# Kernel optimization log

Hardware: AMD Instinct MI355X
Metric: run time of the kernel (lower is better)

The kernel has to match this reference:

```python
import jax, jax.numpy as jnp
import numpy as np

N = 100000
E = 3200000
IN_C, H1, H2 = 512, 64, 32


def gcn_norm(edge_index, edge_weight, num_nodes):
    """PyG gcn_norm with add_self_loops=True: D^-1/2 (A+I) D^-1/2 edge weights."""
    row, col = edge_index[0], edge_index[1]
    loop = jnp.arange(num_nodes, dtype=edge_index.dtype)
    row = jnp.concatenate([row, loop])
    col = jnp.concatenate([col, loop])
    w = jnp.concatenate([edge_weight, jnp.ones((num_nodes,), edge_weight.dtype)])
    deg = jax.ops.segment_sum(w, col, num_segments=num_nodes)
    dinv = jnp.where(deg > 0, jax.lax.rsqrt(jnp.maximum(deg, 1e-12)), 0.0)
    wnorm = dinv[row] * w * dinv[col]
    return row, col, wnorm


def gcn_conv(x, W, b, row, col, wnorm, num_nodes):
    h = x @ W                                   # [N, out] linear first (out <= in)
    msg = wnorm[:, None] * h[row]               # gather + per-edge scale  [E+N, out]
    out = jax.ops.segment_sum(msg, col, num_segments=num_nodes)
    return out + b


def setup_inputs() -> dict:
    key = jax.random.key(0)
    ks = jax.random.split(key, 9)
    x = jax.random.normal(ks[0], (N, IN_C), dtype=jnp.float32)
    edge_index = jax.random.randint(ks[1], (2, E), 0, N, dtype=jnp.int64)
    edge_weight = jax.random.uniform(ks[2], (E,), dtype=jnp.float32)
    # Glorot-style init for GCN linear weights, zero bias (PyG defaults).
    def glorot(k, fan_in, fan_out):
        s = np.sqrt(6.0 / (fan_in + fan_out)).astype(np.float32)
        return jax.random.uniform(k, (fan_in, fan_out), jnp.float32, -s, s)
    return {
        "x": x,
        "edge_index": edge_index,
        "edge_weight": edge_weight,
        "W1": glorot(ks[3], IN_C, H1), "b1": jnp.zeros((H1,), jnp.float32),
        "W2": glorot(ks[4], H1, H2),  "b2": jnp.zeros((H2,), jnp.float32),
        "W3": glorot(ks[5], H2, 1),   "b3": jnp.zeros((1,), jnp.float32),
    }


def reference(x, edge_index, edge_weight, W1, b1, W2, b2, W3, b3):
    # Inference mode: dropout is identity (training=False).
    row, col, wnorm = gcn_norm(edge_index, edge_weight, N)  # cached=True: shared across layers
    h = jax.nn.relu(gcn_conv(x, W1, b1, row, col, wnorm, N))
    h = jax.nn.relu(gcn_conv(h, W2, b2, row, col, wnorm, N))
    h = gcn_conv(h, W3, b3, row, col, wnorm, N)
    return h.reshape(-1)  # [N]
```

## Files before the change

### kernel.cpp

```cpp
#include <hip/hip_runtime.h>

constexpr int BLK = 256;
constexpr int NBLKBIN = 512;
constexpr int MAXNB   = 1024;

typedef __bf16 bf16x8 __attribute__((ext_vector_type(8)));
typedef float  f32x4  __attribute__((ext_vector_type(4)));

__device__ __forceinline__ float blo(unsigned u) { return __uint_as_float(u << 16); }
__device__ __forceinline__ float bhi(unsigned u) { return __uint_as_float(u & 0xffff0000u); }

__device__ __forceinline__ int detect64(const void* ei) {
    const int* p = (const int*)ei;
    int is64 = 1;
#pragma unroll
    for (int i = 0; i < 16; ++i)
        if (p[2 * i + 1] != 0) is64 = 0;
    return is64;
}

__device__ __forceinline__ int load_idx(const void* ei, size_t pos, int is64) {
    if (is64) return (int)((const long long*)ei)[pos];
    return ((const int*)ei)[pos];
}

__global__ void k_prep(const float* __restrict__ W1, const float* __restrict__ W2,
                       __bf16* __restrict__ Wtf, __bf16* __restrict__ Wtf2,
                       int* __restrict__ bkt_cnt, int nb) {
    const int b = blockIdx.x;
    const int t = threadIdx.x;
    if (b < 16) {
        int i = b * 256 + t;
        int lane = i & 63;
        int tt   = (i >> 6) & 3;
        int k0c  = i >> 8;
        int col  = tt * 16 + (lane & 15);
        int kbase = k0c * 32 + (lane >> 4) * 8;
        bf16x8 v;
#pragma unroll
        for (int j = 0; j < 8; ++j) v[j] = (__bf16)W1[(size_t)(kbase + j) * 64 + col];
        *(bf16x8*)(Wtf + (size_t)i * 8) = v;
    } else if (b == 16) {
        int i = t;
        int lane = i & 63;
        int ct   = i >> 6;
        int tt = ct & 1, chunk = ct >> 1;
        int col  = tt * 16 + (lane & 15);
        int kbase = chunk * 32 + (lane >> 4) * 8;
        bf16x8 v;
#pragma unroll
        for (int j = 0; j < 8; ++j) v[j] = (__bf16)W2[(size_t)(kbase + j) * 32 + col];
        *(bf16x8*)(Wtf2 + (size_t)i * 8) = v;
    } else {
        for (int i = t; i < nb; i += 256) bkt_cnt[i] = 0;
    }
}

__global__ __launch_bounds__(256) void k_binhist(const void* __restrict__ ei, int e,
                                                 int* __restrict__ bucket_cnt, int nb) {
    __shared__ int hist[MAXNB];
    const int t = threadIdx.x;
    for (int b = t; b < nb; b += 256) hist[b] = 0;
    __syncthreads();
    const int is64 = detect64(ei);
    const int chunk = (e + NBLKBIN - 1) / NBLKBIN;
    const int i0 = blockIdx.x * chunk;
    const int i1 = min(e, i0 + chunk);
    for (int i = i0 + t; i < i1; i += 256) {
        int dst = load_idx(ei, (size_t)e + i, is64);
        atomicAdd(&hist[dst >> 7], 1);
    }
    __syncthreads();
    for (int b = t; b < nb; b += 256) {
        int c = hist[b];
        if (c) atomicAdd(&bucket_cnt[b], c);
    }
}

__global__ void k_scanbkt(const int* __restrict__ cnt, int* __restrict__ offs,
                          int* __restrict__ cursor, int nb, int e) {
    __shared__ int sh[256];
    const int t = threadIdx.x;
    const int base = t * 4;
    int v[4]; int s = 0;
#pragma unroll
    for (int k = 0; k < 4; ++k) {
        int i = base + k;
        v[k] = (i < nb) ? cnt[i] : 0;
        s += v[k];
    }
    sh[t] = s;
    __syncthreads();
    for (int d = 1; d < 256; d <<= 1) {
        int x = (t >= d) ? sh[t - d] : 0;
        __syncthreads();
        sh[t] += x;
        __syncthreads();
    }
    int excl = (t == 0) ? 0 : sh[t - 1];
#pragma unroll
    for (int k = 0; k < 4; ++k) {
        int i = base + k;
        if (i < nb) { offs[i] = excl; cursor[i] = excl; excl += v[k]; }
    }
    if (t == 255) offs[nb] = e;
}

__global__ __launch_bounds__(256) void k_fat(const void* __restrict__ ei,
                                             const float* __restrict__ ew, int e,
                                             int* __restrict__ bucket_cursor,
                                             int2* __restrict__ binned, int nb,
                                             const float* __restrict__ X,
                                             const __bf16* __restrict__ Wtf,
                                             __bf16* __restrict__ H, int nrows) {
    __shared__ int hist[MAXNB];
    const int t = threadIdx.x;
    if (blockIdx.x < NBLKBIN) {
        for (int b = t; b < nb; b += 256) hist[b] = 0;
        __syncthreads();
        const int is64 = detect64(ei);
        const int chunk = (e + NBLKBIN - 1) / NBLKBIN;
        const int i0 = blockIdx.x * chunk;
        const int i1 = min(e, i0 + chunk);
        for (int i = i0 + t; i < i1; i += 256) {
            int dst = load_idx(ei, (size_t)e + i, is64);
            atomicAdd(&hist[dst >> 7], 1);
        }
        __syncthreads();
        for (int b = t; b < nb; b += 256) {
            int c = hist[b];
            int base = 0;
            if (c) base = atomicAdd(&bucket_cursor[b], c);
            hist[b] = base;
        }
        __syncthreads();
        for (int i = i0 + t; i < i1; i += 256) {
            int dst = load_idx(ei, (size_t)e + i, is64);
            int src = load_idx(ei, (size_t)i, is64);
            float w = ew[i];
            int bin = dst >> 7;
            int pos = atomicAdd(&hist[bin], 1);
            binned[pos] = make_int2(src | ((dst & 127) << 20), __float_as_int(w));
        }
        return;
    }
    const int bid  = blockIdx.x - NBLKBIN;
    const int wave = t >> 6;
    const int lane = t & 63;
    const int l15  = lane & 15;
    const int lq   = lane >> 4;
    const long rbase = (long)bid * 128 + wave * 32;

    long ar0 = rbase + l15;      if (ar0 >= nrows) ar0 = nrows - 1;
    long ar1 = rbase + 16 + l15; if (ar1 >= nrows) ar1 = nrows - 1;
    const float4* x0 = (const float4*)(X + (size_t)ar0 * 512) + lq * 2;
    const float4* x1 = (const float4*)(X + (size_t)ar1 * 512) + lq * 2;

    f32x4 acc[2][4];
#pragma unroll
    for (int r = 0; r < 2; ++r)
#pragma unroll
        for (int tt = 0; tt < 4; ++tt) acc[r][tt] = f32x4{0.f, 0.f, 0.f, 0.f};

    float4 pa[2][2][2];
#pragma unroll
    for (int s = 0; s < 2; ++s) {
        pa[s][0][0] = x0[s * 8]; pa[s][0][1] = x0[s * 8 + 1];
        pa[s][1][0] = x1[s * 8]; pa[s][1][1] = x1[s * 8 + 1];
    }

#pragma unroll
    for (int k0c = 0; k0c < 16; ++k0c) {
        const int s = k0c & 1;
        float4 a00 = pa[s][0][0], a01 = pa[s][0][1];
        float4 a10 = pa[s][1][0], a11 = pa[s][1][1];
        if (k0c + 2 < 16) {
            pa[s][0][0] = x0[(k0c + 2) * 8]; pa[s][0][1] = x0[(k0c + 2) * 8 + 1];
            pa[s][1][0] = x1[(k0c + 2) * 8]; pa[s][1][1] = x1[(k0c + 2) * 8 + 1];
        }
        bf16x8 af0, af1;
        af0[0] = (__bf16)a00.x; af0[1] = (__bf16)a00.y; af0[2] = (__bf16)a00.z; af0[3] = (__bf16)a00.w;
        af0[4] = (__bf16)a01.x; af0[5] = (__bf16)a01.y; af0[6] = (__bf16)a01.z; af0[7] = (__bf16)a01.w;
        af1[0] = (__bf16)a10.x; af1[1] = (__bf16)a10.y; af1[2] = (__bf16)a10.z; af1[3] = (__bf16)a10.w;
        af1[4] = (__bf16)a11.x; af1[5] = (__bf16)a11.y; af1[6] = (__bf16)a11.z; af1[7] = (__bf16)a11.w;
#pragma unroll
        for (int tt = 0; tt < 4; ++tt) {
            bf16x8 bf_ = *(const bf16x8*)(Wtf + ((size_t)(k0c * 4 + tt) * 64 + lane) * 8);
            acc[0][tt] = __builtin_amdgcn_mfma_f32_16x16x32_bf16(af0, bf_, acc[0][tt], 0, 0, 0);
            acc[1][tt] = __builtin_amdgcn_mfma_f32_16x16x32_bf16(af1, bf_, acc[1][tt], 0, 0, 0);
        }
    }
#pragma unroll
    for (int rr = 0; rr < 2; ++rr)
#pragma unroll
    for (int tt = 0; tt < 4; ++tt)
#pragma unroll
    for (int r = 0; r < 4; ++r) {
        long row = rbase + rr * 16 + lq * 4 + r;
        if (row < nrows) H[(size_t)row * 64 + tt * 16 + l15] = (__bf16)acc[rr][tt][r];
    }
}

__global__ __launch_bounds__(256) void k_degoffs(const int* __restrict__ bkt_offs,
                                                 const int2* __restrict__ binned,
                                                 float* __restrict__ dinv,
                                                 int* __restrict__ offs, int n, int e) {
    __shared__ int                icnt[128];
    __shared__ unsigned long long facc[128];
    __shared__ int                scn[128];
    const int t = threadIdx.x;
    const int b = blockIdx.x;
    if (t < 128) { icnt[t] = 0; facc[t] = 0ull; }
    __syncthreads();
    const int j0 = bkt_offs[b], j1 = bkt_offs[b + 1];
    const float SCALE = 1099511627776.f;
    for (int j = j0 + t; j < j1; j += 256) {
        int2 p = binned[j];
        int dl = ((unsigned)p.x) >> 20;
        atomicAdd(&icnt[dl], 1);
        atomicAdd(&facc[dl], (unsigned long long)(__int_as_float(p.y) * SCALE));
    }
    __syncthreads();
    if (t < 128) {
        int nd = b * 128 + t;
        if (nd < n) dinv[nd] = rsqrtf(fmaf((float)facc[t], 1.f / 1099511627776.f, 1.0f));
        scn[t] = icnt[t];
    }
    __syncthreads();
    for (int d = 1; d < 128; d <<= 1) {
        int x = 0;
        if (t < 128 && t >= d) x = scn[t - d];
        __syncthreads();
        if (t < 128) scn[t] += x;
        __syncthreads();
    }
    if (t < 128) {
        int excl = (t == 0) ? 0 : scn[t - 1];
        int nd = b * 128 + t;
        if (nd < n) offs[nd] = j0 + excl;
    }
    if (b == 0 && t == 0) offs[n] = e;
}

__global__ __launch_bounds__(256) void k_place(const int* __restrict__ bkt_offs,
                                               const int2* __restrict__ binned,
                                               const int* __restrict__ offs,
                                               const float* __restrict__ dinv,
                                               int2* __restrict__ csrp, int n) {
    __shared__ int   cur[128];
    __shared__ float ddst[128];
    const int t = threadIdx.x;
    const int b = blockIdx.x;
    if (t < 128) {
        int nd = b * 128 + t;
        cur[t]  = (nd < n) ? offs[nd] : 0;
        ddst[t] = (nd < n) ? dinv[nd] : 0.f;
    }
    __syncthreads();
    const int j0 = bkt_offs[b], j1 = bkt_offs[b + 1];
    for (int j = j0 + t; j < j1; j += 256) {
        int2 p = binned[j];
        int dl  = ((unsigned)p.x) >> 20;
        int src = p.x & 0xFFFFF;
        int pos = atomicAdd(&cur[dl], 1);
        float w2 = __int_as_float(p.y) * dinv[src] * ddst[dl];
        csrp[pos] = make_int2(src, __float_as_int(w2));
    }
}

__global__ __launch_bounds__(256) void k_gemm2_mfma(const __bf16* __restrict__ A,
                                                    const __bf16* __restrict__ Wtf2,
                                                    __bf16* __restrict__ H, int nrows) {
    const int wave = threadIdx.x >> 6;
    const int lane = threadIdx.x & 63;
    const int l15  = lane & 15;
    const int lq   = lane >> 4;
    const long rbase = (long)blockIdx.x * 64 + wave * 16;

    long arow = rbase + l15;
    if (arow >= nrows) arow = nrows - 1;

    f32x4 acc[2] = {{0.f,0.f,0.f,0.f},{0.f,0.f,0.f,0.f}};
#pragma unroll
    for (int c = 0; c < 2; ++c) {
        bf16x8 af = *(const bf16x8*)(A + (size_t)arow * 64 + c * 32 + lq * 8);
#pragma unroll
        for (int t = 0; t < 2; ++t) {
            bf16x8 bf_ = *(const bf16x8*)(Wtf2 + ((size_t)(c * 2 + t) * 64 + lane) * 8);
            acc[t] = __builtin_amdgcn_mfma_f32_16x16x32_bf16(af, bf_, acc[t], 0, 0, 0);
        }
    }
#pragma unroll
    for (int t = 0; t < 2; ++t)
#pragma unroll
    for (int r = 0; r < 4; ++r) {
        long row = rbase + lq * 4 + r;
        if (row < nrows) H[(size_t)row * 32 + t * 16 + l15] = (__bf16)acc[t][r];
    }
}

template <int K, int EPI>
__global__ __launch_bounds__(256) void k_prop_bf(const int* __restrict__ offs,
                                                 const int2* __restrict__ csrp,
                                                 const __bf16* __restrict__ hb,
                                                 const float* __restrict__ dinv,
                                                 const float* __restrict__ bias,
                                                 const float* __restrict__ W3,
                                                 void* __restrict__ outv, int n) {
    constexpr int SUB = K / 4;
    constexpr int NPW = 64 / SUB;
    constexpr int NPB = 4 * NPW;
    const int t    = threadIdx.x;
    const int lane = t & 63;
    const int wave = t >> 6;
    const int chq  = lane & (SUB - 1);
    const int sub  = lane / SUB;
    const long nd  = (long)blockIdx.x * NPB + wave * NPW + sub;
    if (nd >= n) return;

    const unsigned short* h = (const unsigned short*)hb;
    const int j0 = offs[nd], j1 = offs[nd + 1];
    float a0 = 0.f, a1 = 0.f, a2 = 0.f, a3 = 0.f;
    int j = j0;
    for (; j + 3 < j1; j += 4) {
        int2 p0 = csrp[j];
        int2 p1 = csrp[j + 1];
        int2 p2 = csrp[j + 2];
        int2 p3 = csrp[j + 3];
        uint2 u0 = *(const uint2*)(h + (size_t)p0.x * K + 4 * chq);
        uint2 u1 = *(const uint2*)(h + (size_t)p1.x * K + 4 * chq);
        uint2 u2 = *(const uint2*)(h + (size_t)p2.x * K + 4 * chq);
        uint2 u3 = *(const uint2*)(h + (size_t)p3.x * K + 4 * chq);
        float w0 = __int_as_float(p0.y), w1 = __int_as_float(p1.y);
        float w2 = __int_as_float(p2.y), w3 = __int_as_float(p3.y);
        a0 = fmaf(w0, blo(u0.x), a0); a1 = fmaf(w0, bhi(u0.x), a1);
        a2 = fmaf(w0, blo(u0.y), a2); a3 = fmaf(w0, bhi(u0.y), a3);
        a0 = fmaf(w1, blo(u1.x), a0); a1 = fmaf(w1, bhi(u1.x), a1);
        a2 = fmaf(w1, blo(u1.y), a2); a3 = fmaf(w1, bhi(u1.y), a3);
        a0 = fmaf(w2, blo(u2.x), a0); a1 = fmaf(w2, bhi(u2.x), a1);
        a2 = fmaf(w2, blo(u2.y), a2); a3 = fmaf(w2, bhi(u2.y), a3);
        a0 = fmaf(w3, blo(u3.x), a0); a1 = fmaf(w3, bhi(u3.x), a1);
        a2 = fmaf(w3, blo(u3.y), a2); a3 = fmaf(w3, bhi(u3.y), a3);
    }
    for (; j < j1; ++j) {
        int2 p0 = csrp[j];
        uint2 u0 = *(const uint2*)(h + (size_t)p0.x * K + 4 * chq);
        float w0 = __int_as_float(p0.y);
        a0 = fmaf(w0, blo(u0.x), a0); a1 = fmaf(w0, bhi(u0.x), a1);
        a2 = fmaf(w0, blo(u0.y), a2); a3 = fmaf(w0, bhi(u0.y), a3);
    }
    const float di = dinv[nd];
    const float s  = di * di;
    uint2 us = *(const uint2*)(h + (size_t)nd * K + 4 * chq);
    float4 bv = *(const float4*)(bias + 4 * chq);
    float o0 = fmaf(s, blo(us.x), a0 + bv.x);
    float o1 = fmaf(s, bhi(us.x), a1 + bv.y);
    float o2 = fmaf(s, blo(us.y), a2 + bv.z);
    float o3 = fmaf(s, bhi(us.y), a3 + bv.w);
    o0 = fmaxf(o0, 0.f); o1 = fmaxf(o1, 0.f); o2 = fmaxf(o2, 0.f); o3 = fmaxf(o3, 0.f);
    if (EPI == 0) {
        unsigned short s0 = __builtin_bit_cast(unsigned short, (__bf16)o0);
        unsigned short s1 = __builtin_bit_cast(unsigned short, (__bf16)o1);
        unsigned short s2 = __builtin_bit_cast(unsigned short, (__bf16)o2);
        unsigned short s3 = __builtin_bit_cast(unsigned short, (__bf16)o3);
        uint2 pk;
        pk.x = (unsigned)s0 | ((unsigned)s1 << 16);
        pk.y = (unsigned)s2 | ((unsigned)s3 << 16);
        *(uint2*)((unsigned*)outv + (size_t)nd * (K / 2) + 2 * chq) = pk;
    } else {
        float4 wv = *(const float4*)(W3 + 4 * chq);
        float part = o0 * wv.x + o1 * wv.y + o2 * wv.z + o3 * wv.w;
#pragma unroll
        for (int d = SUB / 2; d >= 1; d >>= 1) part += __shfl_xor(part, d, SUB);
        if (chq == 0) ((float*)outv)[nd] = part;
    }
}

__global__ __launch_bounds__(256) void k_prop1(const int* __restrict__ offs,
                                               const int2* __restrict__ csrp,
                                               const float* __restrict__ h,
                                               const float* __restrict__ dinv,
                                               const float* __restrict__ bias,
                                               float* __restrict__ out, int n) {
    long nd = (long)blockIdx.x * BLK + threadIdx.x;
    if (nd >= n) return;
    const int j0 = offs[nd], j1 = offs[nd + 1];
    float acc = 0.f;
    int j = j0;
    for (; j + 3 < j1; j += 4) {
        int2 p0 = csrp[j];
        int2 p1 = csrp[j + 1];
        int2 p2 = csrp[j + 2];
        int2 p3 = csrp[j + 3];
        acc = fmaf(__int_as_float(p0.y), h[p0.x], acc);
        acc = fmaf(__int_as_float(p1.y), h[p1.x], acc);
        acc = fmaf(__int_as_float(p2.y), h[p2.x], acc);
        acc = fmaf(__int_as_float(p3.y), h[p3.x], acc);
    }
    for (; j < j1; ++j) {
        int2 p0 = csrp[j];
        acc = fmaf(__int_as_float(p0.y), h[p0.x], acc);
    }
    const float di = dinv[nd];
    out[nd] = fmaf(di * di, h[nd], acc + bias[0]);
}

extern "C" void kernel_launch(void* const* d_in, const int* in_sizes, int n_in,
                              void* d_out, int out_size, void* d_ws, size_t ws_size,
                              hipStream_t stream) {
    const float* x  = (const float*)d_in[0];
    const void*  ei = d_in[1];
    const float* ew = (const float*)d_in[2];
    const float* W1 = (const float*)d_in[3];
    const float* b1 = (const float*)d_in[4];
    const float* W2 = (const float*)d_in[5];
    const float* b2 = (const float*)d_in[6];
    const float* W3 = (const float*)d_in[7];
    const float* b3 = (const float*)d_in[8];
    float* out = (float*)d_out;

    const int n = in_sizes[0] / 512;
    const int e = in_sizes[2];
    const int nb = (n + 127) >> 7;

    char* ws = (char*)d_ws;
    size_t off = 0;
    auto alloc = [&](size_t bytes) {
        void* p = ws + off;
        off = (off + bytes + 255) & ~(size_t)255;
        return p;
    };
    int2*   binned   = (int2*)  alloc((size_t)e * 8);
    int*    bkt_cnt  = (int*)   alloc((size_t)(MAXNB + 1) * 4);
    int*    bkt_offs = (int*)   alloc((size_t)(MAXNB + 1) * 4);
    int*    bkt_cur  = (int*)   alloc((size_t)(MAXNB + 1) * 4);
    int*    offs     = (int*)   alloc((size_t)(n + 1) * 4);
    int2*   csrp     = (int2*)  alloc((size_t)e * 8);
    float*  dinv     = (float*) alloc((size_t)n * 4);
    __bf16* hb1      = (__bf16*)alloc((size_t)n * 64 * 2);
    __bf16* pb64     = (__bf16*)alloc((size_t)n * 64 * 2);
    __bf16* hbuf2    = (__bf16*)alloc((size_t)n * 32 * 2);
    float*  h3       = (float*) alloc((size_t)n * 4);
    __bf16* Wtf      = (__bf16*)alloc((size_t)512 * 64 * 2);
    __bf16* Wtf2     = (__bf16*)alloc((size_t)64 * 32 * 2);
    (void)ws_size; (void)n_in; (void)out_size;

    const int gb_n = (n + BLK - 1) / BLK;

    k_prep<<<18, 256, 0, stream>>>(W1, W2, Wtf, Wtf2, bkt_cnt, nb);
    k_binhist<<<NBLKBIN, 256, 0, stream>>>(ei, e, bkt_cnt, nb);
    k_scanbkt<<<1, 256, 0, stream>>>(bkt_cnt, bkt_offs, bkt_cur, nb, e);
    k_fat<<<NBLKBIN + (n + 127) / 128, 256, 0, stream>>>(ei, ew, e, bkt_cur, binned, nb,
                                                         x, Wtf, hb1, n);
    k_degoffs<<<nb, 256, 0, stream>>>(bkt_offs, binned, dinv, offs, n, e);
    k_place<<<nb, 256, 0, stream>>>(bkt_offs, binned, offs, dinv, csrp, n);

    k_prop_bf<64, 0><<<(n + 15) / 16, 256, 0, stream>>>(offs, csrp, hb1, dinv, b1, nullptr, pb64, n);
    k_gemm2_mfma<<<(n + 63) / 64, 256, 0, stream>>>(pb64, Wtf2, hbuf2, n);
    k_prop_bf<32, 1><<<(n + 31) / 32, 256, 0, stream>>>(offs, csrp, hbuf2, dinv, b2, W3, h3, n);
    k_prop1<<<gb_n, BLK, 0, stream>>>(offs, csrp, h3, dinv, b3, out, n);
}
```

Baseline: 338.6 us.

## Restructure edge binning pipeline and widen GEMM1 tile to 256 rows

Removes the separate histogram and single-block scan kernels. The fused GEMM kernel's binning blocks now compute per-block histograms and reserve per-block bucket bases with atomics. A new scatter kernel then recomputes the bucket prefix and scatters the edges. k_degoffs and k_place each redo the bucket prefix scan locally instead of reading precomputed offsets. Separately, the first GEMM tile goes from 128 to 256 rows per block (64 rows per wave) for more reuse of W fragments, at the cost of more registers and an extra per-block base table in workspace.

```diff
diff --git a/kernel.cpp b/kernel.cpp
--- a/kernel.cpp
+++ b/kernel.cpp
@@ -56,60 +56,9 @@
     }
 }
 
-__global__ __launch_bounds__(256) void k_binhist(const void* __restrict__ ei, int e,
-                                                 int* __restrict__ bucket_cnt, int nb) {
-    __shared__ int hist[MAXNB];
-    const int t = threadIdx.x;
-    for (int b = t; b < nb; b += 256) hist[b] = 0;
-    __syncthreads();
-    const int is64 = detect64(ei);
-    const int chunk = (e + NBLKBIN - 1) / NBLKBIN;
-    const int i0 = blockIdx.x * chunk;
-    const int i1 = min(e, i0 + chunk);
-    for (int i = i0 + t; i < i1; i += 256) {
-        int dst = load_idx(ei, (size_t)e + i, is64);
-        atomicAdd(&hist[dst >> 7], 1);
-    }
-    __syncthreads();
-    for (int b = t; b < nb; b += 256) {
-        int c = hist[b];
-        if (c) atomicAdd(&bucket_cnt[b], c);
-    }
-}
-
-__global__ void k_scanbkt(const int* __restrict__ cnt, int* __restrict__ offs,
-                          int* __restrict__ cursor, int nb, int e) {
-    __shared__ int sh[256];
-    const int t = threadIdx.x;
-    const int base = t * 4;
-    int v[4]; int s = 0;
-#pragma unroll
-    for (int k = 0; k < 4; ++k) {
-        int i = base + k;
-        v[k] = (i < nb) ? cnt[i] : 0;
-        s += v[k];
-    }
-    sh[t] = s;
-    __syncthreads();
-    for (int d = 1; d < 256; d <<= 1) {
-        int x = (t >= d) ? sh[t - d] : 0;
-        __syncthreads();
-        sh[t] += x;
-        __syncthreads();
-    }
-    int excl = (t == 0) ? 0 : sh[t - 1];
-#pragma unroll
-    for (int k = 0; k < 4; ++k) {
-        int i = base + k;
-        if (i < nb) { offs[i] = excl; cursor[i] = excl; excl += v[k]; }
-    }
-    if (t == 255) offs[nb] = e;
-}
-
-__global__ __launch_bounds__(256) void k_fat(const void* __restrict__ ei,
-                                             const float* __restrict__ ew, int e,
-                                             int* __restrict__ bucket_cursor,
-                                             int2* __restrict__ binned, int nb,
+__global__ __launch_bounds__(256) void k_fat(const void* __restrict__ ei, int e,
+                                             int* __restrict__ bucket_cnt,
+                                             int* __restrict__ blkbase, int nb,
                                              const float* __restrict__ X,
                                              const __bf16* __restrict__ Wtf,
                                              __bf16* __restrict__ H, int nrows) {
@@ -127,20 +76,12 @@
             atomicAdd(&hist[dst >> 7], 1);
         }
         __syncthreads();
+        int* myb = blkbase + (size_t)blockIdx.x * MAXNB;
         for (int b = t; b < nb; b += 256) {
             int c = hist[b];
             int base = 0;
-            if (c) base = atomicAdd(&bucket_cursor[b], c);
-            hist[b] = base;
-        }
-        __syncthreads();
-        for (int i = i0 + t; i < i1; i += 256) {
-            int dst = load_idx(ei, (size_t)e + i, is64);
-            int src = load_idx(ei, (size_t)i, is64);
-            float w = ew[i];
-            int bin = dst >> 7;
-            int pos = atomicAdd(&hist[bin], 1);
-            binned[pos] = make_int2(src | ((dst & 127) << 20), __float_as_int(w));
+            if (c) base = atomicAdd(&bucket_cnt[b], c);
+            myb[b] = base;
         }
         return;
     }
@@ -149,70 +90,160 @@
     const int lane = t & 63;
     const int l15  = lane & 15;
     const int lq   = lane >> 4;
-    const long rbase = (long)bid * 128 + wave * 32;
-
-    long ar0 = rbase + l15;      if (ar0 >= nrows) ar0 = nrows - 1;
-    long ar1 = rbase + 16 + l15; if (ar1 >= nrows) ar1 = nrows - 1;
-    const float4* x0 = (const float4*)(X + (size_t)ar0 * 512) + lq * 2;
-    const float4* x1 = (const float4*)(X + (size_t)ar1 * 512) + lq * 2;
-
-    f32x4 acc[2][4];
-#pragma unroll
-    for (int r = 0; r < 2; ++r)
-#pragma unroll
-        for (int tt = 0; tt < 4; ++tt) acc[r][tt] = f32x4{0.f, 0.f, 0.f, 0.f};
-
-    float4 pa[2][2][2];
-#pragma unroll
-    for (int s = 0; s < 2; ++s) {
-        pa[s][0][0] = x0[s * 8]; pa[s][0][1] = x0[s * 8 + 1];
-        pa[s][1][0] = x1[s * 8]; pa[s][1][1] = x1[s * 8 + 1];
-    }
+    const long rbase = (long)bid * 256 + wave * 64;
+
+    const float4* xr[4];
+#pragma unroll
+    for (int rg = 0; rg < 4; ++rg) {
+        long ar = rbase + rg * 16 + l15;
+        if (ar >= nrows) ar = nrows - 1;
+        xr[rg] = (const float4*)(X + (size_t)ar * 512) + lq * 2;
+    }
+
+    f32x4 acc[4][4];
+#pragma unroll
+    for (int rg = 0; rg < 4; ++rg)
+#pragma unroll
+        for (int tt = 0; tt < 4; ++tt) acc[rg][tt] = f32x4{0.f, 0.f, 0.f, 0.f};
+
+    float4 pa[2][4][2];
+#pragma unroll
+    for (int s = 0; s < 2; ++s)
+#pragma unroll
+        for (int rg = 0; rg < 4; ++rg) {
+            pa[s][rg][0] = xr[rg][s * 8];
+            pa[s][rg][1] = xr[rg][s * 8 + 1];
+        }
 
 #pragma unroll
     for (int k0c = 0; k0c < 16; ++k0c) {
         const int s = k0c & 1;
-        float4 a00 = pa[s][0][0], a01 = pa[s][0][1];
-        float4 a10 = pa[s][1][0], a11 = pa[s][1][1];
+        bf16x8 af[4];
+#pragma unroll
+        for (int rg = 0; rg < 4; ++rg) {
+            float4 a0 = pa[s][rg][0], a1 = pa[s][rg][1];
+            af[rg][0] = (__bf16)a0.x; af[rg][1] = (__bf16)a0.y;
+            af[rg][2] = (__bf16)a0.z; af[rg][3] = (__bf16)a0.w;
+            af[rg][4] = (__bf16)a1.x; af[rg][5] = (__bf16)a1.y;
+            af[rg][6] = (__bf16)a1.z; af[rg][7] = (__bf16)a1.w;
+        }
         if (k0c + 2 < 16) {
-            pa[s][0][0] = x0[(k0c + 2) * 8]; pa[s][0][1] = x0[(k0c + 2) * 8 + 1];
-            pa[s][1][0] = x1[(k0c + 2) * 8]; pa[s][1][1] = x1[(k0c + 2) * 8 + 1];
-        }
-        bf16x8 af0, af1;
-        af0[0] = (__bf16)a00.x; af0[1] = (__bf16)a00.y; af0[2] = (__bf16)a00.z; af0[3] = (__bf16)a00.w;
-        af0[4] = (__bf16)a01.x; af0[5] = (__bf16)a01.y; af0[6] = (__bf16)a01.z; af0[7] = (__bf16)a01.w;
-        af1[0] = (__bf16)a10.x; af1[1] = (__bf16)a10.y; af1[2] = (__bf16)a10.z; af1[3] = (__bf16)a10.w;
-        af1[4] = (__bf16)a11.x; af1[5] = (__bf16)a11.y; af1[6] = (__bf16)a11.z; af1[7] = (__bf16)a11.w;
+#pragma unroll
+            for (int rg = 0; rg < 4; ++rg) {
+                pa[s][rg][0] = xr[rg][(k0c + 2) * 8];
+                pa[s][rg][1] = xr[rg][(k0c + 2) * 8 + 1];
+            }
+        }
 #pragma unroll
         for (int tt = 0; tt < 4; ++tt) {
             bf16x8 bf_ = *(const bf16x8*)(Wtf + ((size_t)(k0c * 4 + tt) * 64 + lane) * 8);
-            acc[0][tt] = __builtin_amdgcn_mfma_f32_16x16x32_bf16(af0, bf_, acc[0][tt], 0, 0, 0);
-            acc[1][tt] = __builtin_amdgcn_mfma_f32_16x16x32_bf16(af1, bf_, acc[1][tt], 0, 0, 0);
-        }
-    }
-#pragma unroll
-    for (int rr = 0; rr < 2; ++rr)
+#pragma unroll
+            for (int rg = 0; rg < 4; ++rg)
+                acc[rg][tt] = __builtin_amdgcn_mfma_f32_16x16x32_bf16(af[rg], bf_, acc[rg][tt], 0, 0, 0);
+        }
+    }
+#pragma unroll
+    for (int rg = 0; rg < 4; ++rg)
 #pragma unroll
     for (int tt = 0; tt < 4; ++tt)
 #pragma unroll
     for (int r = 0; r < 4; ++r) {
-        long row = rbase + rr * 16 + lq * 4 + r;
-        if (row < nrows) H[(size_t)row * 64 + tt * 16 + l15] = (__bf16)acc[rr][tt][r];
-    }
-}
-
-__global__ __launch_bounds__(256) void k_degoffs(const int* __restrict__ bkt_offs,
+        long row = rbase + rg * 16 + lq * 4 + r;
+        if (row < nrows) H[(size_t)row * 64 + tt * 16 + l15] = (__bf16)acc[rg][tt][r];
+    }
+}
+
+__global__ __launch_bounds__(256) void k_binscatter(const void* __restrict__ ei,
+                                                    const float* __restrict__ ew, int e,
+                                                    const int* __restrict__ bkt_cnt,
+                                                    const int* __restrict__ blkbase,
+                                                    int2* __restrict__ binned, int nb) {
+    __shared__ int scn[256];
+    __shared__ int hist[MAXNB];
+    const int t = threadIdx.x;
+    const int base = t * 4;
+    int v[4]; int s = 0;
+#pragma unroll
+    for (int k = 0; k < 4; ++k) {
+        int i = base + k;
+        v[k] = (i < nb) ? bkt_cnt[i] : 0;
+        s += v[k];
+    }
+    scn[t] = s;
+    __syncthreads();
+    for (int d = 1; d < 256; d <<= 1) {
+        int x = (t >= d) ? scn[t - d] : 0;
+        __syncthreads();
+        scn[t] += x;
+        __syncthreads();
+    }
+    int excl = (t == 0) ? 0 : scn[t - 1];
+    const int* myb = blkbase + (size_t)blockIdx.x * MAXNB;
+#pragma unroll
+    for (int k = 0; k < 4; ++k) {
+        int i = base + k;
+        if (i < nb) hist[i] = excl + myb[i];
+        excl += v[k];
+    }
+    __syncthreads();
+    const int is64 = detect64(ei);
+    const int chunk = (e + NBLKBIN - 1) / NBLKBIN;
+    const int i0 = blockIdx.x * chunk;
+    const int i1 = min(e, i0 + chunk);
+    for (int i = i0 + t; i < i1; i += 256) {
+        int dst = load_idx(ei, (size_t)e + i, is64);
+        int src = load_idx(ei, (size_t)i, is64);
+        float w = ew[i];
+        int bin = dst >> 7;
+        int pos = atomicAdd(&hist[bin], 1);
+        binned[pos] = make_int2(src | ((dst & 127) << 20), __float_as_int(w));
+    }
+}
+
+__device__ __forceinline__ void bucket_prefix(const int* __restrict__ bkt_cnt, int nb,
+                                              int* scn, int* pfx) {
+    const int t = threadIdx.x;
+    const int base = t * 4;
+    int v[4]; int s = 0;
+#pragma unroll
+    for (int k = 0; k < 4; ++k) {
+        int i = base + k;
+        v[k] = (i < nb) ? bkt_cnt[i] : 0;
+        s += v[k];
+    }
+    scn[t] = s;
+    __syncthreads();
+    for (int d = 1; d < 256; d <<= 1) {
+        int x = (t >= d) ? scn[t - d] : 0;
+        __syncthreads();
+        scn[t] += x;
+        __syncthreads();
+    }
+    int run = (t == 0) ? 0 : scn[t - 1];
+#pragma unroll
+    for (int k = 0; k < 4; ++k) {
+        run += v[k];
+        pfx[base + k] = run;
+    }
+    __syncthreads();
+}
+
+__global__ __launch_bounds__(256) void k_degoffs(const int* __restrict__ bkt_cnt,
                                                  const int2* __restrict__ binned,
                                                  float* __restrict__ dinv,
-                                                 int* __restrict__ offs, int n, int e) {
+                                                 int* __restrict__ offs, int n, int e, int nb) {
+    __shared__ int                scn[256];
+    __shared__ int                pfx[MAXNB];
     __shared__ int                icnt[128];
     __shared__ unsigned long long facc[128];
-    __shared__ int                scn[128];
+    __shared__ int                scn2[128];
     const int t = threadIdx.x;
     const int b = blockIdx.x;
+    bucket_prefix(bkt_cnt, nb, scn, pfx);
+    const int j0 = (b == 0) ? 0 : pfx[b - 1];
+    const int j1 = pfx[b];
     if (t < 128) { icnt[t] = 0; facc[t] = 0ull; }
     __syncthreads();
-    const int j0 = bkt_offs[b], j1 = bkt_offs[b + 1];
     const float SCALE = 1099511627776.f;
     for (int j = j0 + t; j < j1; j += 256) {
         int2 p = binned[j];
@@ -224,40 +255,44 @@
     if (t < 128) {
         int nd = b * 128 + t;
         if (nd < n) dinv[nd] = rsqrtf(fmaf((float)facc[t], 1.f / 1099511627776.f, 1.0f));
-        scn[t] = icnt[t];
+        scn2[t] = icnt[t];
     }
     __syncthreads();
     for (int d = 1; d < 128; d <<= 1) {
         int x = 0;
-        if (t < 128 && t >= d) x = scn[t - d];
-        __syncthreads();
-        if (t < 128) scn[t] += x;
+        if (t < 128 && t >= d) x = scn2[t - d];
+        __syncthreads();
+        if (t < 128) scn2[t] += x;
         __syncthreads();
     }
     if (t < 128) {
-        int excl = (t == 0) ? 0 : scn[t - 1];
+        int excl = (t == 0) ? 0 : scn2[t - 1];
         int nd = b * 128 + t;
         if (nd < n) offs[nd] = j0 + excl;
     }
     if (b == 0 && t == 0) offs[n] = e;
 }
 
-__global__ __launch_bounds__(256) void k_place(const int* __restrict__ bkt_offs,
+__global__ __launch_bounds__(256) void k_place(const int* __restrict__ bkt_cnt,
                                                const int2* __restrict__ binned,
                                                const int* __restrict__ offs,
                                                const float* __restrict__ dinv,
-                                               int2* __restrict__ csrp, int n) {
+                                               int2* __restrict__ csrp, int n, int nb) {
+    __shared__ int   scn[256];
+    __shared__ int   pfx[MAXNB];
     __shared__ int   cur[128];
     __shared__ float ddst[128];
     const int t = threadIdx.x;
     const int b = blockIdx.x;
+    bucket_prefix(bkt_cnt, nb, scn, pfx);
+    const int j0 = (b == 0) ? 0 : pfx[b - 1];
+    const int j1 = pfx[b];
     if (t < 128) {
         int nd = b * 128 + t;
         cur[t]  = (nd < n) ? offs[nd] : 0;
         ddst[t] = (nd < n) ? dinv[nd] : 0.f;
     }
     __syncthreads();
-    const int j0 = bkt_offs[b], j1 = bkt_offs[b + 1];
     for (int j = j0 + t; j < j1; j += 256) {
         int2 p = binned[j];
         int dl  = ((unsigned)p.x) >> 20;
@@ -432,8 +467,7 @@
     };
     int2*   binned   = (int2*)  alloc((size_t)e * 8);
     int*    bkt_cnt  = (int*)   alloc((size_t)(MAXNB + 1) * 4);
-    int*    bkt_offs = (int*)   alloc((size_t)(MAXNB + 1) * 4);
-    int*    bkt_cur  = (int*)   alloc((size_t)(MAXNB + 1) * 4);
+    int*    blkbase  = (int*)   alloc((size_t)NBLKBIN * MAXNB * 4);
     int*    offs     = (int*)   alloc((size_t)(n + 1) * 4);
     int2*   csrp     = (int2*)  alloc((size_t)e * 8);
     float*  dinv     = (float*) alloc((size_t)n * 4);
@@ -448,12 +482,11 @@
     const int gb_n = (n + BLK - 1) / BLK;
 
     k_prep<<<18, 256, 0, stream>>>(W1, W2, Wtf, Wtf2, bkt_cnt, nb);
-    k_binhist<<<NBLKBIN, 256, 0, stream>>>(ei, e, bkt_cnt, nb);
-    k_scanbkt<<<1, 256, 0, stream>>>(bkt_cnt, bkt_offs, bkt_cur, nb, e);
-    k_fat<<<NBLKBIN + (n + 127) / 128, 256, 0, stream>>>(ei, ew, e, bkt_cur, binned, nb,
+    k_fat<<<NBLKBIN + (n + 255) / 256, 256, 0, stream>>>(ei, e, bkt_cnt, blkbase, nb,
                                                          x, Wtf, hb1, n);
-    k_degoffs<<<nb, 256, 0, stream>>>(bkt_offs, binned, dinv, offs, n, e);
-    k_place<<<nb, 256, 0, stream>>>(bkt_offs, binned, offs, dinv, csrp, n);
+    k_binscatter<<<NBLKBIN, 256, 0, stream>>>(ei, ew, e, bkt_cnt, blkbase, binned, nb);
+    k_degoffs<<<nb, 256, 0, stream>>>(bkt_cnt, binned, dinv, offs, n, e, nb);
+    k_place<<<nb, 256, 0, stream>>>(bkt_cnt, binned, offs, dinv, csrp, n, nb);
 
     k_prop_bf<64, 0><<<(n + 15) / 16, 256, 0, stream>>>(offs, csrp, hb1, dinv, b1, nullptr, pb64, n);
     k_gemm2_mfma<<<(n + 63) / 64, 256, 0, stream>>>(pb64, Wtf2, hbuf2, n);
```

Measured after the change: 346.5 us. +2.3%, slower.
